# Kernel tuning notes

Measured on AMD Instinct MI355X. Metric: run time of the kernel, lower is better.

## Reference

```python
import jax, jax.numpy as jnp
import numpy as np

# Config constants (mirror MoEConfig)
NUM_EXPERTS = 8
TOP_K = 2
CAPACITY_FACTOR = 1.25
TEMPERATURE = 1.0
LB_LOSS_WEIGHT = 0.01


def setup_inputs() -> dict:
    key = jax.random.key(0)
    k1, k2 = jax.random.split(key)
    B, S, H = 8, 4096, 1024
    hidden_states = jax.random.normal(k1, (B, S, H), dtype=jnp.float32)
    # nn.Linear weight, init std=0.02, no bias
    router_w = jax.random.normal(k2, (NUM_EXPERTS, H), dtype=jnp.float32) * 0.02
    return {"hidden_states": hidden_states, "router_w": router_w}


def _token_choice_routing(hidden_states, router_w):
    B, S, H = hidden_states.shape
    E = router_w.shape[0]
    N = B * S

    # Router (eval mode: no noise since noise_epsilon=0)
    router_logits = jnp.einsum('bsh,eh->bse', hidden_states, router_w) / TEMPERATURE
    router_probs = jax.nn.softmax(router_logits, axis=-1)

    # Top-k expert selection per token, renormalize weights
    expert_weights, expert_indices = jax.lax.top_k(router_probs, TOP_K)  # [B,S,K]
    expert_weights = expert_weights / expert_weights.sum(axis=-1, keepdims=True)

    # Scatter into dispatch mask [B,S,E] (top-k indices are unique per token)
    one_hot = jax.nn.one_hot(expert_indices, E, dtype=expert_weights.dtype)  # [B,S,K,E]
    dispatch_mask = jnp.einsum('bske,bsk->bse', one_hot, expert_weights)

    tokens_per_expert = dispatch_mask.sum(axis=(0, 1))  # [E]

    # Auxiliary load-balance loss
    expert_fraction = tokens_per_expert / N
    mean_prob = router_probs.mean(axis=(0, 1))
    load_balancing_loss = N * jnp.sum(expert_fraction * mean_prob) * LB_LOSS_WEIGHT

    # Capacity constraint: keep only top-`capacity` weights per expert over all tokens
    capacity = int(CAPACITY_FACTOR * S * B / E)
    flat = dispatch_mask.reshape(N, E).T  # [E, N]
    vals, idx = jax.lax.top_k(flat, capacity)  # [E, capacity]
    new_flat = jnp.zeros_like(flat).at[jnp.arange(E)[:, None], idx].set(vals)
    constrained = new_flat.T.reshape(B, S, E)
    # torch code only rewrites experts that exceed capacity
    over = tokens_per_expert > capacity  # [E]
    dispatch_mask = jnp.where(over, constrained, dispatch_mask)

    return dispatch_mask, load_balancing_loss, router_probs


def reference(hidden_states, router_w):
    dispatch_mask, lb_loss, router_probs = _token_choice_routing(hidden_states, router_w)
    # combine_weights == dispatch_mask in the original module
    return dispatch_mask, lb_loss, router_probs
```

## Files before the change

kernel.cpp:

```cpp
#include <hip/hip_runtime.h>

#define H 1024
#define E 8
#define BLK 256
#define CAP 5120
#define FBLK 1024

typedef float f32x4 __attribute__((ext_vector_type(4)));

__global__ __launch_bounds__(BLK, 5) void router_kernel(
    const float* __restrict__ hs,
    const float* __restrict__ rw,
    float* __restrict__ dispatch,
    float* __restrict__ probs_out,
    float* __restrict__ partial)
{
    __shared__ float w_lds[E * H];

    const int tid  = threadIdx.x;
    const int wave = tid >> 6;
    const int lane = tid & 63;
    const int t    = lane >> 4;
    const int f    = lane & 15;
    const int wid  = blockIdx.x * (BLK / 64) + wave;
    const size_t tok0 = (size_t)wid * 8 + t * 2;
    const float* h0 = hs + tok0 * H + 4 * f;

    f32x4 A0[2], A1[2];
#pragma unroll
    for (int j = 0; j < 2; ++j) {
        A0[j] = *(const f32x4*)(h0 + j * 64);
        A1[j] = *(const f32x4*)(h0 + H + j * 64);
    }

    for (int i = tid; i < E * H / 4; i += BLK)
        ((f32x4*)w_lds)[i] = ((const f32x4*)rw)[i];
    __syncthreads();

    float acc0[E], acc1[E];
#pragma unroll
    for (int e = 0; e < E; ++e) { acc0[e] = 0.f; acc1[e] = 0.f; }

#pragma unroll
    for (int c = 0; c < 16; ++c) {
        const f32x4 a0 = A0[c & 1], a1 = A1[c & 1];
        if (c < 14) {
            A0[c & 1] = *(const f32x4*)(h0 + (c + 2) * 64);
            A1[c & 1] = *(const f32x4*)(h0 + H + (c + 2) * 64);
        }
        const float* wb = w_lds + c * 64 + 4 * f;
#pragma unroll
        for (int eg = 0; eg < 2; ++eg) {
            f32x4 wv[4];
#pragma unroll
            for (int q = 0; q < 4; ++q)
                wv[q] = *(const f32x4*)(wb + (eg * 4 + q) * H);
#pragma unroll
            for (int q = 0; q < 4; ++q) {
                const int e = eg * 4 + q;
                acc0[e] = fmaf(a0[0], wv[q][0], acc0[e]);
                acc0[e] = fmaf(a0[1], wv[q][1], acc0[e]);
                acc0[e] = fmaf(a0[2], wv[q][2], acc0[e]);
                acc0[e] = fmaf(a0[3], wv[q][3], acc0[e]);
                acc1[e] = fmaf(a1[0], wv[q][0], acc1[e]);
                acc1[e] = fmaf(a1[1], wv[q][1], acc1[e]);
                acc1[e] = fmaf(a1[2], wv[q][2], acc1[e]);
                acc1[e] = fmaf(a1[3], wv[q][3], acc1[e]);
            }
        }
    }

#pragma unroll
    for (int e = 0; e < E; ++e) {
        float v0 = acc0[e], v1 = acc1[e];
        v0 += __shfl_xor(v0, 1); v1 += __shfl_xor(v1, 1);
        v0 += __shfl_xor(v0, 2); v1 += __shfl_xor(v1, 2);
        v0 += __shfl_xor(v0, 4); v1 += __shfl_xor(v1, 4);
        v0 += __shfl_xor(v0, 8); v1 += __shfl_xor(v1, 8);
        acc0[e] = v0; acc1[e] = v1;
    }

    const int se = f & 7;
    const int sk = f >> 3;
    float slotv = 0.f;

#pragma unroll
    for (int j = 0; j < 2; ++j) {
        const float* L = j ? acc1 : acc0;
        float mx = L[0];
#pragma unroll
        for (int e = 1; e < E; ++e) mx = fmaxf(mx, L[e]);
        float p[E], s = 0.f;
#pragma unroll
        for (int e = 0; e < E; ++e) { p[e] = expf(L[e] - mx); s += p[e]; }
        const float inv = 1.f / s;
#pragma unroll
        for (int e = 0; e < E; ++e) p[e] *= inv;

        int i1 = 0;
#pragma unroll
        for (int e = 1; e < E; ++e) if (p[e] > p[i1]) i1 = e;
        int i2 = -1;
#pragma unroll
        for (int e = 0; e < E; ++e) {
            if (e == i1) continue;
            if (i2 < 0 || p[e] > p[i2]) i2 = e;
        }
        const float s12 = p[i1] + p[i2];
        const float w1 = p[i1] / s12;
        const float w2 = p[i2] / s12;

        const size_t tok = tok0 + j;
        if (f < 8) {
            const float de = (f == i1) ? w1 : ((f == i2) ? w2 : 0.f);
            dispatch[tok * E + f] = de;
        } else {
            probs_out[tok * E + (f - 8)] = p[f - 8];
        }
        slotv += sk ? p[se] : ((se == i1) ? w1 : ((se == i2) ? w2 : 0.f));
    }

    __syncthreads();
    float* red = w_lds;
    red[wave * 64 + lane] = slotv;
    __syncthreads();
    if (tid < 16) {
        float s = 0.f;
#pragma unroll
        for (int k = 0; k < 16; ++k) s += red[k * 16 + tid];
        partial[(size_t)tid * gridDim.x + blockIdx.x] = s;
    }
}

__global__ __launch_bounds__(FBLK) void finalize_kernel(
    float* __restrict__ dispatch,
    const float* __restrict__ partial,
    int nb,
    float* __restrict__ lb_out,
    int N)
{
    const int e    = blockIdx.x;
    const int tid  = threadIdx.x;
    const int lane = tid & 63;
    const int wv   = tid >> 6;

    __shared__ float g[16];
    {
        float v = 0.f;
        for (int b = lane; b < nb; b += 64) v += partial[(size_t)wv * nb + b];
#pragma unroll
        for (int off = 32; off; off >>= 1) v += __shfl_xor(v, off);
        if (lane == 0) g[wv] = v;
    }
    __syncthreads();

    if (e == 0 && tid == 0) {
        float s = 0.f;
        for (int i = 0; i < E; ++i) s += g[i] * g[E + i];
        *lb_out = 0.01f * s / (float)N;
    }

    const float tpe = g[e];
    if (!(tpe > (float)CAP)) return;

    __shared__ unsigned hist[256];
    __shared__ unsigned sh_prefix;
    __shared__ int sh_k;

    unsigned prefix = 0;
    int k = CAP;

    for (int round = 0; round < 4; ++round) {
        const int shift = 24 - 8 * round;
        for (int i = tid; i < 256; i += FBLK) hist[i] = 0;
        __syncthreads();
        const unsigned mhi = (round == 0) ? 0u : (0xFFFFFFFFu << (shift + 8));
        for (int i = tid; i < N; i += FBLK) {
            const unsigned bits = __float_as_uint(dispatch[(size_t)i * E + e]);
            if ((bits & mhi) == (prefix & mhi))
                atomicAdd(&hist[(bits >> shift) & 255u], 1u);
        }
        __syncthreads();
        if (tid == 0) {
            int cum = 0;
            int d = 255;
            for (; d > 0; --d) {
                const int h = (int)hist[d];
                if (cum + h >= k) break;
                cum += h;
            }
            sh_prefix = prefix | ((unsigned)d << shift);
            sh_k = k - cum;
        }
        __syncthreads();
        prefix = sh_prefix;
        k = sh_k;
        __syncthreads();
    }

    const unsigned T = prefix;
    const unsigned r = (unsigned)k;

    __shared__ unsigned wave_cnt[FBLK / 64];
    __shared__ unsigned running;
    if (tid == 0) running = 0;
    __syncthreads();

    for (int base = 0; base < N; base += FBLK) {
        const int i = base + tid;
        const unsigned bits = __float_as_uint(dispatch[(size_t)i * E + e]);
        const bool eq = (bits == T);
        const unsigned long long bal = __ballot(eq);
        if (lane == 0) wave_cnt[wv] = (unsigned)__popcll(bal);
        __syncthreads();
        unsigned before = running;
        for (int w = 0; w < wv; ++w) before += wave_cnt[w];
        const unsigned rank = before + (unsigned)__popcll(bal & ((1ull << lane) - 1ull));
        const bool keep = (bits > T) || (eq && rank < r);
        if (!keep) dispatch[(size_t)i * E + e] = 0.f;
        __syncthreads();
        if (tid == 0) {
            unsigned tot = 0;
            for (int w = 0; w < FBLK / 64; ++w) tot += wave_cnt[w];
            running += tot;
        }
        __syncthreads();
    }
}

extern "C" void kernel_launch(void* const* d_in, const int* in_sizes, int n_in,
                              void* d_out, int out_size, void* d_ws, size_t ws_size,
                              hipStream_t stream)
{
    const float* hs = (const float*)d_in[0];
    const float* rw = (const float*)d_in[1];
    const int n_tokens = in_sizes[0] / H;

    float* dispatch = (float*)d_out;
    float* lb       = dispatch + (size_t)n_tokens * E;
    float* probs    = lb + 1;
    float* partial  = (float*)d_ws;

    const int nb = n_tokens / 32;
    router_kernel<<<nb, BLK, 0, stream>>>(hs, rw, dispatch, probs, partial);
    finalize_kernel<<<E, FBLK, 0, stream>>>(dispatch, partial, nb, lb, n_tokens);
}
```

Measured before the change: 205.7 us.

## Keep router weights in registers and process sixteen tokens per wave

```diff
diff --git a/kernel.cpp b/kernel.cpp
--- a/kernel.cpp
+++ b/kernel.cpp
@@ -5,130 +5,140 @@
 #define BLK 256
 #define CAP 5120
 #define FBLK 1024
+#define TPW 16
 
 typedef float f32x4 __attribute__((ext_vector_type(4)));
 
-__global__ __launch_bounds__(BLK, 5) void router_kernel(
+__global__ __launch_bounds__(BLK, 2) void router_kernel(
     const float* __restrict__ hs,
     const float* __restrict__ rw,
     float* __restrict__ dispatch,
     float* __restrict__ probs_out,
     float* __restrict__ partial)
 {
-    __shared__ float w_lds[E * H];
+    __shared__ float red[4][16][16];
 
     const int tid  = threadIdx.x;
     const int wave = tid >> 6;
     const int lane = tid & 63;
-    const int t    = lane >> 4;
-    const int f    = lane & 15;
-    const int wid  = blockIdx.x * (BLK / 64) + wave;
-    const size_t tok0 = (size_t)wid * 8 + t * 2;
-    const float* h0 = hs + tok0 * H + 4 * f;
-
-    f32x4 A0[2], A1[2];
-#pragma unroll
-    for (int j = 0; j < 2; ++j) {
-        A0[j] = *(const f32x4*)(h0 + j * 64);
-        A1[j] = *(const f32x4*)(h0 + H + j * 64);
-    }
-
-    for (int i = tid; i < E * H / 4; i += BLK)
-        ((f32x4*)w_lds)[i] = ((const f32x4*)rw)[i];
-    __syncthreads();
-
-    float acc0[E], acc1[E];
-#pragma unroll
-    for (int e = 0; e < E; ++e) { acc0[e] = 0.f; acc1[e] = 0.f; }
-
-#pragma unroll
-    for (int c = 0; c < 16; ++c) {
-        const f32x4 a0 = A0[c & 1], a1 = A1[c & 1];
-        if (c < 14) {
-            A0[c & 1] = *(const f32x4*)(h0 + (c + 2) * 64);
-            A1[c & 1] = *(const f32x4*)(h0 + H + (c + 2) * 64);
-        }
-        const float* wb = w_lds + c * 64 + 4 * f;
-#pragma unroll
-        for (int eg = 0; eg < 2; ++eg) {
-            f32x4 wv[4];
-#pragma unroll
-            for (int q = 0; q < 4; ++q)
-                wv[q] = *(const f32x4*)(wb + (eg * 4 + q) * H);
+    const size_t tok0 = ((size_t)blockIdx.x * (BLK / 64) + wave) * TPW;
+    const float* h0 = hs + tok0 * H + 4 * lane;
+
+    f32x4 A0[4], A1[4];
+#pragma unroll
+    for (int q = 0; q < 4; ++q) A0[q] = *(const f32x4*)(h0 + q * 256);
+#pragma unroll
+    for (int q = 0; q < 4; ++q) A1[q] = *(const f32x4*)(h0 + H + q * 256);
+
+    f32x4 w[E][4];
+#pragma unroll
+    for (int e = 0; e < E; ++e)
+#pragma unroll
+        for (int q = 0; q < 4; ++q)
+            w[e][q] = *(const f32x4*)(rw + e * H + q * 256 + 4 * lane);
+
+    float mylog[E];
+#pragma unroll
+    for (int e = 0; e < E; ++e) mylog[e] = 0.f;
+
+    const float* pnext = h0 + 2 * H;
+
+#pragma unroll 1
+    for (int t = 0; t < TPW; t += 2) {
+        float acc0[E], acc1[E];
+#pragma unroll
+        for (int e = 0; e < E; ++e) { acc0[e] = 0.f; acc1[e] = 0.f; }
+
+#pragma unroll
+        for (int e = 0; e < E; ++e)
 #pragma unroll
             for (int q = 0; q < 4; ++q) {
-                const int e = eg * 4 + q;
-                acc0[e] = fmaf(a0[0], wv[q][0], acc0[e]);
-                acc0[e] = fmaf(a0[1], wv[q][1], acc0[e]);
-                acc0[e] = fmaf(a0[2], wv[q][2], acc0[e]);
-                acc0[e] = fmaf(a0[3], wv[q][3], acc0[e]);
-                acc1[e] = fmaf(a1[0], wv[q][0], acc1[e]);
-                acc1[e] = fmaf(a1[1], wv[q][1], acc1[e]);
-                acc1[e] = fmaf(a1[2], wv[q][2], acc1[e]);
-                acc1[e] = fmaf(a1[3], wv[q][3], acc1[e]);
+                acc0[e] = fmaf(A0[q][0], w[e][q][0], acc0[e]);
+                acc0[e] = fmaf(A0[q][1], w[e][q][1], acc0[e]);
+                acc0[e] = fmaf(A0[q][2], w[e][q][2], acc0[e]);
+                acc0[e] = fmaf(A0[q][3], w[e][q][3], acc0[e]);
             }
-        }
-    }
-
+        if (t + 2 < TPW) {
+#pragma unroll
+            for (int q = 0; q < 4; ++q) A0[q] = *(const f32x4*)(pnext + q * 256);
+        }
+
+#pragma unroll
+        for (int e = 0; e < E; ++e)
+#pragma unroll
+            for (int q = 0; q < 4; ++q) {
+                acc1[e] = fmaf(A1[q][0], w[e][q][0], acc1[e]);
+                acc1[e] = fmaf(A1[q][1], w[e][q][1], acc1[e]);
+                acc1[e] = fmaf(A1[q][2], w[e][q][2], acc1[e]);
+                acc1[e] = fmaf(A1[q][3], w[e][q][3], acc1[e]);
+            }
+        if (t + 3 < TPW) {
+#pragma unroll
+            for (int q = 0; q < 4; ++q) A1[q] = *(const f32x4*)(pnext + H + q * 256);
+        }
+        pnext += 2 * H;
+
+#pragma unroll
+        for (int e = 0; e < E; ++e) {
+            float v0 = acc0[e], v1 = acc1[e];
+            v0 += __shfl_xor(v0, 1);  v1 += __shfl_xor(v1, 1);
+            v0 += __shfl_xor(v0, 2);  v1 += __shfl_xor(v1, 2);
+            v0 += __shfl_xor(v0, 4);  v1 += __shfl_xor(v1, 4);
+            v0 += __shfl_xor(v0, 8);  v1 += __shfl_xor(v1, 8);
+            v0 += __shfl_xor(v0, 16); v1 += __shfl_xor(v1, 16);
+            v0 += __shfl_xor(v0, 32); v1 += __shfl_xor(v1, 32);
+            mylog[e] = (lane == t)     ? v0 : mylog[e];
+            mylog[e] = (lane == t + 1) ? v1 : mylog[e];
+        }
+    }
+
+    float mx = mylog[0];
+#pragma unroll
+    for (int e = 1; e < E; ++e) mx = fmaxf(mx, mylog[e]);
+    float p[E], s = 0.f;
+#pragma unroll
+    for (int e = 0; e < E; ++e) { p[e] = expf(mylog[e] - mx); s += p[e]; }
+    const float inv = 1.f / s;
+#pragma unroll
+    for (int e = 0; e < E; ++e) p[e] *= inv;
+
+    int i1 = 0; float v1 = p[0];
+#pragma unroll
+    for (int e = 1; e < E; ++e) if (p[e] > v1) { v1 = p[e]; i1 = e; }
+    int i2 = -1; float v2 = -1.f;
 #pragma unroll
     for (int e = 0; e < E; ++e) {
-        float v0 = acc0[e], v1 = acc1[e];
-        v0 += __shfl_xor(v0, 1); v1 += __shfl_xor(v1, 1);
-        v0 += __shfl_xor(v0, 2); v1 += __shfl_xor(v1, 2);
-        v0 += __shfl_xor(v0, 4); v1 += __shfl_xor(v1, 4);
-        v0 += __shfl_xor(v0, 8); v1 += __shfl_xor(v1, 8);
-        acc0[e] = v0; acc1[e] = v1;
-    }
-
-    const int se = f & 7;
-    const int sk = f >> 3;
-    float slotv = 0.f;
-
-#pragma unroll
-    for (int j = 0; j < 2; ++j) {
-        const float* L = j ? acc1 : acc0;
-        float mx = L[0];
-#pragma unroll
-        for (int e = 1; e < E; ++e) mx = fmaxf(mx, L[e]);
-        float p[E], s = 0.f;
-#pragma unroll
-        for (int e = 0; e < E; ++e) { p[e] = expf(L[e] - mx); s += p[e]; }
-        const float inv = 1.f / s;
-#pragma unroll
-        for (int e = 0; e < E; ++e) p[e] *= inv;
-
-        int i1 = 0;
-#pragma unroll
-        for (int e = 1; e < E; ++e) if (p[e] > p[i1]) i1 = e;
-        int i2 = -1;
-#pragma unroll
-        for (int e = 0; e < E; ++e) {
-            if (e == i1) continue;
-            if (i2 < 0 || p[e] > p[i2]) i2 = e;
-        }
-        const float s12 = p[i1] + p[i2];
-        const float w1 = p[i1] / s12;
-        const float w2 = p[i2] / s12;
-
-        const size_t tok = tok0 + j;
-        if (f < 8) {
-            const float de = (f == i1) ? w1 : ((f == i2) ? w2 : 0.f);
-            dispatch[tok * E + f] = de;
-        } else {
-            probs_out[tok * E + (f - 8)] = p[f - 8];
-        }
-        slotv += sk ? p[se] : ((se == i1) ? w1 : ((se == i2) ? w2 : 0.f));
-    }
-
-    __syncthreads();
-    float* red = w_lds;
-    red[wave * 64 + lane] = slotv;
+        if (e == i1) continue;
+        if (p[e] > v2) { v2 = p[e]; i2 = e; }
+    }
+    const float s12 = v1 + v2;
+    const float w1 = v1 / s12;
+    const float w2 = v2 / s12;
+
+    float d[E];
+#pragma unroll
+    for (int e = 0; e < E; ++e)
+        d[e] = (e == i1) ? w1 : ((e == i2) ? w2 : 0.f);
+
+    f32x4 dv0 = {d[0], d[1], d[2], d[3]}, dv1 = {d[4], d[5], d[6], d[7]};
+    f32x4 pv0 = {p[0], p[1], p[2], p[3]}, pv1 = {p[4], p[5], p[6], p[7]};
+
+    if (lane < TPW) {
+        const size_t tok = tok0 + lane;
+        *(f32x4*)(dispatch  + tok * E)     = dv0;
+        *(f32x4*)(dispatch  + tok * E + 4) = dv1;
+        *(f32x4*)(probs_out + tok * E)     = pv0;
+        *(f32x4*)(probs_out + tok * E + 4) = pv1;
+        f32x4* dst = (f32x4*)&red[wave][lane][0];
+        dst[0] = dv0; dst[1] = dv1; dst[2] = pv0; dst[3] = pv1;
+    }
     __syncthreads();
     if (tid < 16) {
-        float s = 0.f;
-#pragma unroll
-        for (int k = 0; k < 16; ++k) s += red[k * 16 + tid];
-        partial[(size_t)tid * gridDim.x + blockIdx.x] = s;
+        float acc = 0.f;
+#pragma unroll
+        for (int wv = 0; wv < 4; ++wv)
+            for (int l = 0; l < TPW; ++l) acc += red[wv][l][tid];
+        partial[(size_t)tid * gridDim.x + blockIdx.x] = acc;
     }
 }
 
@@ -241,7 +251,7 @@
     float* probs    = lb + 1;
     float* partial  = (float*)d_ws;
 
-    const int nb = n_tokens / 32;
+    const int nb = n_tokens / (4 * TPW);
     router_kernel<<<nb, BLK, 0, stream>>>(hs, rw, dispatch, probs, partial);
     finalize_kernel<<<E, FBLK, 0, stream>>>(dispatch, partial, nb, lb, n_tokens);
 }
```

After: 263.1 us. 1.28x slower.
